# Kernel optimization log

Hardware: AMD Instinct MI355X
Metric: run time of the kernel (lower is better)

## Reference

```python
import jax, jax.numpy as jnp
import numpy as np


def haar_level(x):
    """One 2D Haar (periodization-equivalent for even sizes) DWT on [B,K,C,H,W].
    Returns [B,4K,C,H/2,W/2] with per-parent band order (LL, Hx, Hy, Hxy),
    matching the tree's append order yl, yh0, yh1, yh2."""
    B, K, C, H, W = x.shape
    x = x.reshape(B, K, C, H // 2, 2, W // 2, 2)
    a = x[:, :, :, :, 0, :, 0]
    b = x[:, :, :, :, 0, :, 1]
    c = x[:, :, :, :, 1, :, 0]
    d = x[:, :, :, :, 1, :, 1]
    ll = (a + b + c + d) * 0.5
    h1 = (a - b + c - d) * 0.5   # high along width
    h2 = (a + b - c - d) * 0.5   # high along height
    h3 = (a - b - c + d) * 0.5   # diagonal
    out = jnp.stack([ll, h1, h2, h3], axis=2)  # [B,K,4,C,H/2,W/2]
    return out.reshape(B, 4 * K, C, H // 2, W // 2)


def conv2d(x, w, b, stride, pad):
    y = jax.lax.conv_general_dilated(
        x, w, window_strides=(stride, stride),
        padding=[(pad, pad), (pad, pad)],
        dimension_numbers=('NCHW', 'OIHW', 'NCHW'))
    return y + b[None, :, None, None]


def setup_inputs() -> dict:
    key = jax.random.key(0)
    ks = jax.random.split(key, 9)
    s = 0.05
    return {
        'x':        jax.random.normal(ks[0], (64, 3, 224, 224), dtype=jnp.float32),
        'w_s1':     jax.random.normal(ks[1], (192, 3, 7, 7), dtype=jnp.float32) * s,
        'b_s1':     jax.random.normal(ks[2], (192,), dtype=jnp.float32) * s,
        'w_s2':     jax.random.normal(ks[3], (192, 192, 7, 7), dtype=jnp.float32) * s,
        'b_s2':     jax.random.normal(ks[4], (192,), dtype=jnp.float32) * s,
        'w_p':      jax.random.normal(ks[5], (768, 960, 3, 3), dtype=jnp.float32) * s,
        'b_p':      jax.random.normal(ks[6], (768,), dtype=jnp.float32) * s,
        'cls_token': jax.random.normal(ks[7], (1, 1, 768), dtype=jnp.float32),
        'positions': jax.random.normal(ks[8], (50, 768), dtype=jnp.float32),
    }


def reference(x, w_s1, b_s1, w_s2, b_s2, w_p, b_p, cls_token, positions):
    B = x.shape[0]
    # ---- 4-level full Haar wavelet packet tree (vectorized over subbands) ----
    t = x[:, None]                      # [B,1,3,224,224]
    for _ in range(4):
        t = haar_level(t)               # -> [B,256,3,14,14]
    wav = t.reshape(B, 256 * 3, 14, 14)  # [B,768,14,14] (tree concat order)
    # ---- spatial branch: two strided 7x7 convs (224 -> 56 -> 14) ----
    sp = conv2d(x, w_s1, b_s1, stride=4, pad=3)
    sp = conv2d(sp, w_s2, b_s2, stride=4, pad=3)   # [B,192,14,14]
    feat = jnp.concatenate([wav, sp], axis=1)      # [B,960,14,14]
    # ---- patch projection conv 3x3 s2 -> 7x7, flatten to tokens ----
    y = conv2d(feat, w_p, b_p, stride=2, pad=1)    # [B,768,7,7]
    y = y.reshape(B, 768, 49).transpose(0, 2, 1)   # [B,49,768]
    cls = jnp.broadcast_to(cls_token, (B, 1, 768))
    y = jnp.concatenate([cls, y], axis=1) + positions  # [B,50,768]
    return y
```

## Files before the change

### kernel.cpp

```cpp
#include <hip/hip_runtime.h>
#include <stdint.h>

typedef __attribute__((ext_vector_type(8))) short short8;
typedef __attribute__((ext_vector_type(4))) float floatx4;

__device__ inline unsigned short f2bf(float f){
  union { float fv; unsigned int u; } v; v.fv = f;
  unsigned int u = v.u;
  unsigned int r = ((u >> 16) & 1u) + 0x7FFFu;
  return (unsigned short)((u + r) >> 16);
}

__device__ __forceinline__ void async16(const void* g, void* l){
  __builtin_amdgcn_global_load_lds(
      (const __attribute__((address_space(1))) unsigned int*)g,
      (__attribute__((address_space(3))) unsigned int*)l, 16, 0, 0);
}

#define PBAR(N) do {                                              \
    asm volatile("s_waitcnt vmcnt(" #N ")" ::: "memory");          \
    __builtin_amdgcn_s_barrier();                                  \
    asm volatile("" ::: "memory");                                 \
  } while (0)

__global__ void prep_w1(const float* __restrict__ w, unsigned short* __restrict__ w1p){
  int i = blockIdx.x*256 + threadIdx.x;
  if (i >= 192*192) return;
  int k = i % 192, o = i / 192;
  int cc = k >> 3, kx = k & 7;
  unsigned short v = 0;
  if (cc < 21 && kx < 7){
    int c = cc / 7, ky = cc % 7;
    v = f2bf(w[(o*3 + c)*49 + ky*7 + kx]);
  }
  w1p[i] = v;
}
__global__ void prep_w2(const float* __restrict__ w, unsigned short* __restrict__ w2p){
  int i = blockIdx.x*256 + threadIdx.x;
  if (i >= 192*9408) return;
  int k = i % 9408, o = i / 9408;
  int g = k / 192, c = k % 192;
  int ky = g / 7, kx = g % 7;
  w2p[i] = f2bf(w[((o*192 + c)*7 + ky)*7 + kx]);
}
__global__ void prep_w3(const float* __restrict__ w, unsigned short* __restrict__ w3p){
  int i = blockIdx.x*256 + threadIdx.x;
  if (i >= 768*8640) return;
  int k = i % 8640, o = i / 8640;
  int g = k / 960, c = k % 960;
  int ky = g / 3, kx = g % 3;
  w3p[i] = f2bf(w[((o*960 + c)*3 + ky)*3 + kx]);
}
__global__ void prep_zp(unsigned int* __restrict__ zp){
  zp[threadIdx.x] = 0u;
}
__global__ void zero_f32(float* __restrict__ p, int n){
  int i = blockIdx.x*256 + threadIdx.x;
  if (i < n) p[i] = 0.f;
}

__global__ void pad_x2(const float* __restrict__ x, unsigned short* __restrict__ xh2){
  int idx = blockIdx.x*256 + threadIdx.x;
  if (idx >= 64*3*230*56*8) return;
  int kx = idx & 7; int t = idx >> 3;
  int ox = t % 56;  t /= 56;
  int iy = t % 230; t /= 230;
  int row = iy - 3;
  int col = 4*ox - 3 + kx;
  unsigned short v = 0;
  if (row >= 0 && row < 224 && col >= 0 && col < 224)
    v = f2bf(x[((size_t)t*224 + row)*224 + col]);
  xh2[idx] = v;
}

__global__ void wavelet_kernel(const float* __restrict__ x, unsigned short* __restrict__ feat){
  int blk = blockIdx.x;
  int j = blk % 14; blk /= 14;
  int i = blk % 14; blk /= 14;
  int c = blk % 3;  int b = blk / 3;
  int t = threadIdx.x;
  int u = t >> 4, v = t & 15;
  float val = x[((size_t)(b*3 + c)*224 + (i*16 + u))*224 + (j*16 + v)];
  #pragma unroll
  for (int bit = 1; bit < 64; bit <<= 1){
    float p = __shfl_xor(val, bit);
    val = (t & bit) ? (p - val) : (val + p);
  }
  __shared__ float s[256];
  #pragma unroll
  for (int bit = 64; bit < 256; bit <<= 1){
    s[t] = val; __syncthreads();
    float p = s[t ^ bit]; __syncthreads();
    val = (t & bit) ? (p - val) : (val + p);
  }
  s[t] = val; __syncthreads();
  int k = t;
  int d1 = (k>>6)&3, d2 = (k>>4)&3, d3 = (k>>2)&3, d4 = k&3;
  int mr = (d1>>1) | ((d2>>1)<<1) | ((d3>>1)<<2) | ((d4>>1)<<3);
  int mc = (d1&1)  | ((d2&1)<<1)  | ((d3&1)<<2)  | ((d4&1)<<3);
  float outv = s[mr*16 + mc] * 0.0625f;
  feat[((size_t)((b*14 + i)*14 + j))*960 + (k*3 + c)] = f2bf(outv);
}

__global__ __launch_bounds__(256) void conv1_gemm(const unsigned short* __restrict__ xh2,
                                                  const unsigned short* __restrict__ w1p,
                                                  const float* __restrict__ b1,
                                                  unsigned short* __restrict__ sp1){
  __shared__ unsigned short As[2][128*64], Bs[2][64*64];
  int m0 = blockIdx.x*128, n0 = blockIdx.y*64;
  int tid = threadIdx.x, wave = tid >> 6, lane = tid & 63;
  int l16 = lane & 15, quad = lane >> 4;
  int wy = wave >> 1, wx = wave & 1;
  int r8 = lane >> 3, kb = (lane & 7) ^ r8;

  int Abase[4];
  #pragma unroll
  for (int j = 0; j < 4; j++){
    int row = wave*32 + j*8 + r8;
    int m = m0 + row;
    int ox = m % 56; int t = m / 56; int oy = t % 56; int b = t / 56;
    Abase[j] = (b*690 + 4*oy)*448 + ox*8;
  }
  const unsigned short* pB0 = w1p + (n0 + wave*16 + r8)*192 + kb*8;
  const unsigned short* pB1 = pB0 + 8*192;

  int sw = l16 & 7;
  int xo0 = ((quad    ) ^ sw)*8;
  int xo1 = ((quad + 4) ^ sw)*8;
  int aoff[4];
  #pragma unroll
  for (int mt = 0; mt < 4; mt++) aoff[mt] = (wy*64 + mt*16 + l16)*64;
  int boff0 = (wx*32 + l16)*64, boff1 = boff0 + 16*64;

  floatx4 acc[4][2];
  #pragma unroll
  for (int mt = 0; mt < 4; mt++)
    #pragma unroll
    for (int nt = 0; nt < 2; nt++) acc[mt][nt] = (floatx4){0.f,0.f,0.f,0.f};

  auto stage = [&](int i, int buf){
    int cc = i*8 + kb;
    int c = (cc*147) >> 10;
    int ky = cc - 7*c;
    int koff = (c*230 + ky)*448;
    #pragma unroll
    for (int j = 0; j < 4; j++)
      async16(xh2 + Abase[j] + koff, (void*)&As[buf][(wave*32 + j*8)*64]);
    async16(pB0 + i*64, (void*)&Bs[buf][(wave*16    )*64]);
    async16(pB1 + i*64, (void*)&Bs[buf][(wave*16 + 8)*64]);
  };

  stage(0, 0);
  __syncthreads();
  #pragma unroll
  for (int i = 0; i < 3; i++){
    int buf = i & 1;
    if (i < 2) stage(i+1, buf ^ 1);
    #pragma unroll
    for (int ks = 0; ks < 2; ks++){
      int xo = ks ? xo1 : xo0;
      short8 b0 = *(const short8*)&Bs[buf][boff0 + xo];
      short8 b1 = *(const short8*)&Bs[buf][boff1 + xo];
      #pragma unroll
      for (int mt = 0; mt < 4; mt++){
        short8 a = *(const short8*)&As[buf][aoff[mt] + xo];
        acc[mt][0] = __builtin_amdgcn_mfma_f32_16x16x32_bf16(a, b0, acc[mt][0], 0, 0, 0);
        acc[mt][1] = __builtin_amdgcn_mfma_f32_16x16x32_bf16(a, b1, acc[mt][1], 0, 0, 0);
      }
    }
    __syncthreads();
  }

  #pragma unroll
  for (int mt = 0; mt < 4; mt++){
    #pragma unroll
    for (int rg = 0; rg < 4; rg++){
      int row = wy*64 + mt*16 + quad*4 + rg;
      size_t ob = (size_t)(m0 + row)*192;
      #pragma unroll
      for (int nt = 0; nt < 2; nt++){
        int nn = n0 + wx*32 + nt*16 + l16;
        sp1[ob + nn] = f2bf(acc[mt][nt][rg] + b1[nn]);
      }
    }
  }
}

template<int MODE>
__global__ __launch_bounds__(256) void conv_split(const unsigned short* __restrict__ Ain,
                                                  const unsigned short* __restrict__ Bt,
                                                  const unsigned short* __restrict__ zp,
                                                  float* __restrict__ pout){
  constexpr int OH  = (MODE==2) ? 14 : 7;
  constexpr int OW  = OH;
  constexpr int IH  = (MODE==2) ? 56 : 14;
  constexpr int IW  = IH;
  constexpr int Cin = (MODE==2) ? 192 : 960;
  constexpr int KW  = (MODE==2) ? 7 : 3;
  constexpr int S   = (MODE==2) ? 4 : 2;
  constexpr int P   = (MODE==2) ? 3 : 1;
  constexpr int K   = (MODE==2) ? 9408 : 8640;
  constexpr int K3  = K/3;
  constexpr int NB  = K3/64;
  constexpr int MTI = (MODE==2) ? 98 : 25;
  constexpr int NTI = (MODE==2) ? 2 : 8;
  constexpr int M   = (MODE==2) ? 12544 : 3136;
  constexpr int NF  = (MODE==2) ? 192 : 768;

  int id = blockIdx.x;
  int mtile = id % MTI;
  int kn = id / MTI;
  int kseg = kn / NTI, ntile = kn % NTI;
  int m0 = mtile*128, n0 = ntile*96;

  __shared__ unsigned short As[2][128*64], Bs[2][96*64];
  int tid = threadIdx.x, wv = tid >> 6, lane = tid & 63;
  int l16 = lane & 15, quad = lane >> 4;
  int wy = wv >> 1, wx = wv & 1;
  int r8 = lane >> 3, kb = (lane & 7) ^ r8;
  int sw = l16 & 7;

  int abase[4], iyb[4], ixb[4];
  #pragma unroll
  for (int j = 0; j < 4; j++){
    int r = wv*32 + j*8 + r8;
    int m = m0 + r; if (m > M-1) m = M-1;
    int ox = m % OW; int t = m / OW; int oy = t % OH; int bb = t / OH;
    iyb[j] = S*oy - P; ixb[j] = S*ox - P;
    abase[j] = ((bb*IH + iyb[j])*IW + ixb[j])*Cin + kb*8;
  }
  const unsigned short* pB[3];
  #pragma unroll
  for (int j = 0; j < 3; j++)
    pB[j] = Bt + (size_t)(n0 + wv*24 + j*8 + r8)*K + kseg*K3 + kb*8;

  int k0 = kseg*K3;
  int c0 = k0 % Cin;
  int gk = k0 / Cin;
  int kx = gk % KW, ky = gk / KW;
  int k0n = 0;

  floatx4 acc[4][3];
  #pragma unroll
  for (int mt = 0; mt < 4; mt++)
    #pragma unroll
    for (int nt = 0; nt < 3; nt++) acc[mt][nt] = (floatx4){0.f,0.f,0.f,0.f};

  auto stage = [&](int buf){
    int koff = (ky*IW + kx)*Cin + c0;
    #pragma unroll
    for (int j = 0; j < 4; j++){
      int iy = iyb[j] + ky, ix = ixb[j] + kx;
      const unsigned short* pa = ((unsigned)iy < (unsigned)IH && (unsigned)ix < (unsigned)IW)
                                 ? (Ain + abase[j] + koff) : zp;
      async16(pa, (void*)&As[buf][(wv*32 + j*8)*64]);
    }
    #pragma unroll
    for (int j = 0; j < 3; j++)
      async16(pB[j] + k0n, (void*)&Bs[buf][(wv*24 + j*8)*64]);
    k0n += 64;
    c0 += 64;
    if (c0 == Cin){ c0 = 0; kx++; if (kx == KW){ kx = 0; ky++; } }
  };

  auto compute = [&](int buf){
    #pragma unroll
    for (int ks = 0; ks < 2; ks++){
      int xo = ((ks*4 + quad) ^ sw)*8;
      short8 b0 = *(const short8*)&Bs[buf][(wx*48      + l16)*64 + xo];
      short8 b1 = *(const short8*)&Bs[buf][(wx*48 + 16 + l16)*64 + xo];
      short8 b2 = *(const short8*)&Bs[buf][(wx*48 + 32 + l16)*64 + xo];
      #pragma unroll
      for (int mt = 0; mt < 4; mt++){
        short8 a = *(const short8*)&As[buf][(wy*64 + mt*16 + l16)*64 + xo];
        acc[mt][0] = __builtin_amdgcn_mfma_f32_16x16x32_bf16(a, b0, acc[mt][0], 0, 0, 0);
        acc[mt][1] = __builtin_amdgcn_mfma_f32_16x16x32_bf16(a, b1, acc[mt][1], 0, 0, 0);
        acc[mt][2] = __builtin_amdgcn_mfma_f32_16x16x32_bf16(a, b2, acc[mt][2], 0, 0, 0);
      }
    }
  };

  stage(0);
  PBAR(0);
  for (int i = 0; i < NB; i++){
    if (i + 1 < NB) stage((i+1) & 1);
    compute(i & 1);
    PBAR(0);
  }

  #pragma unroll
  for (int mt = 0; mt < 4; mt++){
    #pragma unroll
    for (int rg = 0; rg < 4; rg++){
      int row = wy*64 + mt*16 + quad*4 + rg;
      int mm = m0 + row;
      #pragma unroll
      for (int nt = 0; nt < 3; nt++){
        int nn = n0 + wx*48 + nt*16 + l16;
        atomicAdd(&pout[(size_t)mm*NF + nn], acc[mt][nt][rg]);
      }
    }
  }
}

__global__ void comb2(const float* __restrict__ pc, const float* __restrict__ bias,
                      unsigned short* __restrict__ feat){
  int i = blockIdx.x*256 + threadIdx.x;
  int n = i % 192, m = i / 192;
  feat[(size_t)m*960 + 768 + n] = f2bf(pc[i] + bias[n]);
}
__global__ void comb3(const float* __restrict__ pc, const float* __restrict__ bias,
                      const float* __restrict__ pos, float* __restrict__ out){
  int i = blockIdx.x*256 + threadIdx.x;
  int n = i % 768, m = i / 768;
  int b2 = m / 49, tt = m - b2*49;
  float v = pc[(size_t)m*768 + n] + bias[n] + pos[(size_t)(1 + tt)*768 + n];
  out[((size_t)(m + b2 + 1))*768 + n] = v;
}

__global__ void cls_kernel(const float* __restrict__ cls, const float* __restrict__ pos,
                           float* __restrict__ out){
  int i = blockIdx.x*256 + threadIdx.x;
  if (i >= 64*768) return;
  int e = i % 768, b = i / 768;
  out[(size_t)(b*50)*768 + e] = cls[e] + pos[e];
}

extern "C" void kernel_launch(void* const* d_in, const int* in_sizes, int n_in,
                              void* d_out, int out_size, void* d_ws, size_t ws_size,
                              hipStream_t stream){
  (void)in_sizes; (void)n_in; (void)out_size;
  const float* x    = (const float*)d_in[0];
  const float* w_s1 = (const float*)d_in[1];
  const float* b_s1 = (const float*)d_in[2];
  const float* w_s2 = (const float*)d_in[3];
  const float* b_s2 = (const float*)d_in[4];
  const float* w_p  = (const float*)d_in[5];
  const float* b_p  = (const float*)d_in[6];
  const float* cls  = (const float*)d_in[7];
  const float* pos  = (const float*)d_in[8];
  float* out = (float*)d_out;

  char* ws = (char*)d_ws;
  if (ws_size < 118235136u) return;
  unsigned short* w1p  = (unsigned short*)(ws + 0);
  unsigned short* sp1  = (unsigned short*)(ws + 131072);
  unsigned short* zp   = (unsigned short*)(ws + 77201408u);
  unsigned short* w2p  = (unsigned short*)(ws + 77266944u);
  unsigned short* w3p  = (unsigned short*)(ws + 80879616u);
  unsigned short* feat = (unsigned short*)(ws + 94150656u);
  unsigned short* xh2  = (unsigned short*)(ws + 77266944u);
  float* pc2 = (float*)(ws + 80879616u);
  float* pc3 = (float*)(ws + 131072);

  prep_w1<<<(192*192 + 255)/256, 256, 0, stream>>>(w_s1, w1p);
  pad_x2<<<(64*3*230*56*8)/256, 256, 0, stream>>>(x, xh2);
  conv1_gemm<<<dim3(1568, 3), 256, 0, stream>>>(xh2, w1p, b_s1, sp1);
  prep_w2<<<(192*9408 + 255)/256, 256, 0, stream>>>(w_s2, w2p);
  prep_zp<<<1, 64, 0, stream>>>((unsigned int*)zp);
  wavelet_kernel<<<64*3*14*14, 256, 0, stream>>>(x, feat);

  zero_f32<<<9408, 256, 0, stream>>>(pc2, 12544*192);
  conv_split<2><<<588, 256, 0, stream>>>(sp1, w2p, zp, pc2);
  comb2<<<9408, 256, 0, stream>>>(pc2, b_s2, feat);

  prep_w3<<<(768*8640 + 255)/256, 256, 0, stream>>>(w_p, w3p);
  zero_f32<<<9600, 256, 0, stream>>>(pc3, 3200*768);
  conv_split<3><<<600, 256, 0, stream>>>(feat, w3p, zp, pc3);
  comb3<<<9408, 256, 0, stream>>>(pc3, b_p, pos, out);
  cls_kernel<<<(64*768 + 255)/256, 256, 0, stream>>>(cls, pos, out);
}
```

Before: 486.9 us.

## Retile split-K conv GEMMs with 128x64 tiles, BK=32, triple-buffered async loads

```diff
diff --git a/kernel.cpp b/kernel.cpp
--- a/kernel.cpp
+++ b/kernel.cpp
@@ -187,7 +187,7 @@
 }
 
 template<int MODE>
-__global__ __launch_bounds__(256) void conv_split(const unsigned short* __restrict__ Ain,
+__global__ __launch_bounds__(256, 4) void conv_ks(const unsigned short* __restrict__ Ain,
                                                   const unsigned short* __restrict__ Bt,
                                                   const unsigned short* __restrict__ zp,
                                                   float* __restrict__ pout){
@@ -200,93 +200,103 @@
   constexpr int S   = (MODE==2) ? 4 : 2;
   constexpr int P   = (MODE==2) ? 3 : 1;
   constexpr int K   = (MODE==2) ? 9408 : 8640;
-  constexpr int K3  = K/3;
-  constexpr int NB  = K3/64;
+  constexpr int K2  = K/2;
+  constexpr int NB  = K2/32;
   constexpr int MTI = (MODE==2) ? 98 : 25;
-  constexpr int NTI = (MODE==2) ? 2 : 8;
+  constexpr int NTI = (MODE==2) ? 3 : 12;
+  constexpr int GRP = 8*NTI;
+  constexpr int PERSEG = (MODE==2) ? 13*GRP : 4*GRP;
   constexpr int M   = (MODE==2) ? 12544 : 3136;
   constexpr int NF  = (MODE==2) ? 192 : 768;
 
   int id = blockIdx.x;
-  int mtile = id % MTI;
-  int kn = id / MTI;
-  int kseg = kn / NTI, ntile = kn % NTI;
-  int m0 = mtile*128, n0 = ntile*96;
-
-  __shared__ unsigned short As[2][128*64], Bs[2][96*64];
+  int kseg = id / PERSEG; int rem = id % PERSEG;
+  int g = rem / GRP, r2 = rem % GRP;
+  int mtile = g*8 + (r2 & 7);
+  if (mtile >= MTI) return;
+  int ntile = r2 >> 3;
+  int m0 = mtile*128, n0 = ntile*64;
+
+  __shared__ unsigned short As[3][4096], Bs[3][2048];
+
   int tid = threadIdx.x, wv = tid >> 6, lane = tid & 63;
   int l16 = lane & 15, quad = lane >> 4;
   int wy = wv >> 1, wx = wv & 1;
-  int r8 = lane >> 3, kb = (lane & 7) ^ r8;
-  int sw = l16 & 7;
-
-  int abase[4], iyb[4], ixb[4];
-  #pragma unroll
-  for (int j = 0; j < 4; j++){
-    int r = wv*32 + j*8 + r8;
-    int m = m0 + r; if (m > M-1) m = M-1;
+
+  int rl = lane >> 2;
+  int go = ((lane & 3) ^ ((lane >> 3) & 3))*8;
+
+  int iyb[2], ixb[2], abase[2];
+  #pragma unroll
+  for (int j = 0; j < 2; j++){
+    int r = (wv + j*4)*16 + rl;
+    int m = m0 + r; if (MODE == 3 && m > M-1) m = M-1;
     int ox = m % OW; int t = m / OW; int oy = t % OH; int bb = t / OH;
     iyb[j] = S*oy - P; ixb[j] = S*ox - P;
-    abase[j] = ((bb*IH + iyb[j])*IW + ixb[j])*Cin + kb*8;
-  }
-  const unsigned short* pB[3];
-  #pragma unroll
-  for (int j = 0; j < 3; j++)
-    pB[j] = Bt + (size_t)(n0 + wv*24 + j*8 + r8)*K + kseg*K3 + kb*8;
-
-  int k0 = kseg*K3;
+    abase[j] = ((bb*IH + iyb[j])*IW + ixb[j])*Cin + go;
+  }
+  const unsigned short* pB = Bt + (size_t)(n0 + wv*16 + rl)*K + kseg*K2 + go;
+
+  int k0 = kseg*K2;
   int c0 = k0 % Cin;
   int gk = k0 / Cin;
-  int kx = gk % KW, ky = gk / KW;
+  int ky = gk / KW, kx = gk % KW;
   int k0n = 0;
 
-  floatx4 acc[4][3];
+  int xo = (quad ^ ((l16 >> 1) & 3))*8;
+
+  floatx4 acc[4][2];
   #pragma unroll
   for (int mt = 0; mt < 4; mt++)
     #pragma unroll
-    for (int nt = 0; nt < 3; nt++) acc[mt][nt] = (floatx4){0.f,0.f,0.f,0.f};
+    for (int nt = 0; nt < 2; nt++) acc[mt][nt] = (floatx4){0.f,0.f,0.f,0.f};
 
   auto stage = [&](int buf){
     int koff = (ky*IW + kx)*Cin + c0;
     #pragma unroll
-    for (int j = 0; j < 4; j++){
+    for (int j = 0; j < 2; j++){
       int iy = iyb[j] + ky, ix = ixb[j] + kx;
       const unsigned short* pa = ((unsigned)iy < (unsigned)IH && (unsigned)ix < (unsigned)IW)
                                  ? (Ain + abase[j] + koff) : zp;
-      async16(pa, (void*)&As[buf][(wv*32 + j*8)*64]);
+      async16(pa, (void*)&As[buf][(wv + j*4)*512]);
     }
-    #pragma unroll
-    for (int j = 0; j < 3; j++)
-      async16(pB[j] + k0n, (void*)&Bs[buf][(wv*24 + j*8)*64]);
-    k0n += 64;
-    c0 += 64;
+    async16(pB + k0n, (void*)&Bs[buf][wv*512]);
+    k0n += 32;
+    c0 += 32;
     if (c0 == Cin){ c0 = 0; kx++; if (kx == KW){ kx = 0; ky++; } }
   };
 
   auto compute = [&](int buf){
-    #pragma unroll
-    for (int ks = 0; ks < 2; ks++){
-      int xo = ((ks*4 + quad) ^ sw)*8;
-      short8 b0 = *(const short8*)&Bs[buf][(wx*48      + l16)*64 + xo];
-      short8 b1 = *(const short8*)&Bs[buf][(wx*48 + 16 + l16)*64 + xo];
-      short8 b2 = *(const short8*)&Bs[buf][(wx*48 + 32 + l16)*64 + xo];
-      #pragma unroll
-      for (int mt = 0; mt < 4; mt++){
-        short8 a = *(const short8*)&As[buf][(wy*64 + mt*16 + l16)*64 + xo];
-        acc[mt][0] = __builtin_amdgcn_mfma_f32_16x16x32_bf16(a, b0, acc[mt][0], 0, 0, 0);
-        acc[mt][1] = __builtin_amdgcn_mfma_f32_16x16x32_bf16(a, b1, acc[mt][1], 0, 0, 0);
-        acc[mt][2] = __builtin_amdgcn_mfma_f32_16x16x32_bf16(a, b2, acc[mt][2], 0, 0, 0);
-      }
-    }
+    short8 b0 = *(const short8*)&Bs[buf][(wx*32      + l16)*32 + xo];
+    short8 b1 = *(const short8*)&Bs[buf][(wx*32 + 16 + l16)*32 + xo];
+    short8 a0 = *(const short8*)&As[buf][(wy*64       + l16)*32 + xo];
+    short8 a1 = *(const short8*)&As[buf][(wy*64 + 16  + l16)*32 + xo];
+    short8 a2 = *(const short8*)&As[buf][(wy*64 + 32  + l16)*32 + xo];
+    short8 a3 = *(const short8*)&As[buf][(wy*64 + 48  + l16)*32 + xo];
+    acc[0][0] = __builtin_amdgcn_mfma_f32_16x16x32_bf16(a0, b0, acc[0][0], 0, 0, 0);
+    acc[0][1] = __builtin_amdgcn_mfma_f32_16x16x32_bf16(a0, b1, acc[0][1], 0, 0, 0);
+    acc[1][0] = __builtin_amdgcn_mfma_f32_16x16x32_bf16(a1, b0, acc[1][0], 0, 0, 0);
+    acc[1][1] = __builtin_amdgcn_mfma_f32_16x16x32_bf16(a1, b1, acc[1][1], 0, 0, 0);
+    acc[2][0] = __builtin_amdgcn_mfma_f32_16x16x32_bf16(a2, b0, acc[2][0], 0, 0, 0);
+    acc[2][1] = __builtin_amdgcn_mfma_f32_16x16x32_bf16(a2, b1, acc[2][1], 0, 0, 0);
+    acc[3][0] = __builtin_amdgcn_mfma_f32_16x16x32_bf16(a3, b0, acc[3][0], 0, 0, 0);
+    acc[3][1] = __builtin_amdgcn_mfma_f32_16x16x32_bf16(a3, b1, acc[3][1], 0, 0, 0);
   };
 
-  stage(0);
+  stage(0); stage(1);
+  int bc = 0;
+  for (int i = 0; i < NB - 2; i++){
+    PBAR(3);
+    int bn = bc + 2; if (bn >= 3) bn -= 3;
+    stage(bn);
+    compute(bc);
+    bc = (bc == 2) ? 0 : bc + 1;
+  }
+  PBAR(3);
+  compute(bc);
+  bc = (bc == 2) ? 0 : bc + 1;
   PBAR(0);
-  for (int i = 0; i < NB; i++){
-    if (i + 1 < NB) stage((i+1) & 1);
-    compute(i & 1);
-    PBAR(0);
-  }
+  compute(bc);
 
   #pragma unroll
   for (int mt = 0; mt < 4; mt++){
@@ -294,9 +304,10 @@
     for (int rg = 0; rg < 4; rg++){
       int row = wy*64 + mt*16 + quad*4 + rg;
       int mm = m0 + row;
+      if (MODE == 3 && mm >= M) continue;
       #pragma unroll
-      for (int nt = 0; nt < 3; nt++){
-        int nn = n0 + wx*48 + nt*16 + l16;
+      for (int nt = 0; nt < 2; nt++){
+        int nn = n0 + wx*32 + nt*16 + l16;
         atomicAdd(&pout[(size_t)mm*NF + nn], acc[mt][nt][rg]);
       }
     }
@@ -361,12 +372,12 @@
   wavelet_kernel<<<64*3*14*14, 256, 0, stream>>>(x, feat);
 
   zero_f32<<<9408, 256, 0, stream>>>(pc2, 12544*192);
-  conv_split<2><<<588, 256, 0, stream>>>(sp1, w2p, zp, pc2);
+  conv_ks<2><<<624, 256, 0, stream>>>(sp1, w2p, zp, pc2);
   comb2<<<9408, 256, 0, stream>>>(pc2, b_s2, feat);
 
   prep_w3<<<(768*8640 + 255)/256, 256, 0, stream>>>(w_p, w3p);
   zero_f32<<<9600, 256, 0, stream>>>(pc3, 3200*768);
-  conv_split<3><<<600, 256, 0, stream>>>(feat, w3p, zp, pc3);
+  conv_ks<3><<<768, 256, 0, stream>>>(feat, w3p, zp, pc3);
   comb3<<<9408, 256, 0, stream>>>(pc3, b_p, pos, out);
   cls_kernel<<<(64*768 + 255)/256, 256, 0, stream>>>(cls, pos, out);
 }
```

After: 457.3 us. -6.1%, faster.
